# Optimization experiments

Measured on AMD Instinct MI355X. Metric: run time of the kernel, lower is better.

## Reference

```python
import jax, jax.numpy as jnp
import numpy as np

B, N, E = 8, 2048, 65536
NUM_RADIAL, H = 6, 128


def setup_inputs() -> dict:
    key = jax.random.key(0)
    ks = jax.random.split(key, 10)
    x = jax.random.normal(ks[0], (B, N, 1), dtype=jnp.float32)
    rbf = jax.random.normal(ks[1], (B, E, NUM_RADIAL), dtype=jnp.float32)
    i = jax.random.randint(ks[2], (E,), 0, N, dtype=jnp.int64)
    j = jax.random.randint(ks[3], (E,), 0, N, dtype=jnp.int64)
    # params (torch Linear convention: w [out, in], y = x @ w.T + b)
    emb_w = jax.random.uniform(ks[4], (H, 1), dtype=jnp.float32, minval=-np.sqrt(3), maxval=np.sqrt(3))
    emb_b = jax.random.normal(ks[5], (H,), dtype=jnp.float32) * 0.1
    rbf_w = jax.random.normal(ks[6], (H, NUM_RADIAL), dtype=jnp.float32) * (1.0 / np.sqrt(NUM_RADIAL))
    rbf_b = jax.random.normal(ks[7], (H,), dtype=jnp.float32) * 0.1
    lin_w = jax.random.normal(ks[8], (H, 3 * H), dtype=jnp.float32) * (1.0 / np.sqrt(3 * H))
    lin_b = jax.random.normal(ks[9], (H,), dtype=jnp.float32) * 0.1
    return {"x": x, "rbf": rbf, "i": i, "j": j,
            "emb_w": emb_w, "emb_b": emb_b,
            "rbf_w": rbf_w, "rbf_b": rbf_b,
            "lin_w": lin_w, "lin_b": lin_b}


def reference(x, rbf, i, j, emb_w, emb_b, rbf_w, rbf_b, lin_w, lin_b):
    act = jax.nn.silu
    # node embedding: [B, N, 1] -> [B, N, H]
    h = x @ emb_w.T + emb_b
    # rbf projection: [B, E, num_radial] -> [B, E, H]
    r = act(rbf @ rbf_w.T + rbf_b)
    # gather per-edge node features and concat: [B, E, 3H]
    cat = jnp.concatenate([h[:, i], h[:, j], r], axis=-1)
    # output: [B, E, H]
    return act(cat @ lin_w.T + lin_b)
```

## Files before the change

### kernel.cpp

```cpp
#include <hip/hip_runtime.h>

#define NB 8
#define NNODE 2048
#define NEDGE 65536
#define H 128
#define BM 64
#define RSTRIDE 132

typedef __attribute__((ext_vector_type(8))) short bf16x8;
typedef __attribute__((ext_vector_type(4))) float f32x4;

union U8 { uint4 u4; bf16x8 s8; };

__device__ __forceinline__ unsigned f32_bf16_rne(float f) {
    unsigned u = __float_as_uint(f);
    return (u + 0x7FFFu + ((u >> 16) & 1u)) >> 16;
}
__device__ __forceinline__ float bf16_f32(unsigned h) {
    return __uint_as_float(h << 16);
}
__device__ __forceinline__ float silu_f(float a) {
    return a / (1.0f + __expf(-a));
}

__global__ __launch_bounds__(64) void precomp_kernel(
    const float* __restrict__ emb_w, const float* __restrict__ emb_b,
    const float* __restrict__ lin_w, const float* __restrict__ lin_b,
    float* __restrict__ ws)
{
    const int bid = blockIdx.x;
    const int t = threadIdx.x;
    if (bid < 32) {
        const int ks = bid >> 3, nt = bid & 7;
        const int g = t >> 4, c = t & 15;
        const int col = nt * 16 + c;
        const float* src = lin_w + col * 384 + 256;
        uint4 w;
        {
            int k0 = ks * 32 + g * 8;
            w.x = f32_bf16_rne(src[k0 + 0]) | (f32_bf16_rne(src[k0 + 1]) << 16);
            w.y = f32_bf16_rne(src[k0 + 2]) | (f32_bf16_rne(src[k0 + 3]) << 16);
            w.z = f32_bf16_rne(src[k0 + 4]) | (f32_bf16_rne(src[k0 + 5]) << 16);
            w.w = f32_bf16_rne(src[k0 + 6]) | (f32_bf16_rne(src[k0 + 7]) << 16);
        }
        unsigned* w3f = (unsigned*)(ws + 384);
        *(uint4*)(w3f + bid * 256 + t * 4) = w;
    } else {
        const int o = (bid - 32) * 64 + t;
        const float* wrow = lin_w + o * 384;
        float u1 = 0.f, u2 = 0.f, v = lin_b[o];
        #pragma unroll 8
        for (int c = 0; c < 128; ++c) {
            float w1 = wrow[c], w2 = wrow[128 + c];
            u1 += emb_w[c] * w1;
            u2 += emb_w[c] * w2;
            v  += emb_b[c] * (w1 + w2);
        }
        ws[o] = u1; ws[128 + o] = u2; ws[256 + o] = v;
    }
}

__global__ __launch_bounds__(256, 4) void edge_kernel(
    const float* __restrict__ x,
    const float* __restrict__ rbf,
    const int*   __restrict__ gi,
    const int*   __restrict__ gj,
    const float* __restrict__ rbf_w,
    const float* __restrict__ rbf_b,
    const float* __restrict__ ws,
    float* __restrict__ out)
{
    __shared__ unsigned RHL[BM * RSTRIDE];
    __shared__ float rbf_s[BM * 6];

    const int tid  = threadIdx.x;
    const int wid  = tid >> 6;
    const int lane = tid & 63;
    const int g    = lane >> 4;
    const int c15  = lane & 15;
    const long m0  = (long)blockIdx.x * BM;

    if (tid < 96)
        ((float4*)rbf_s)[tid] = ((const float4*)(rbf + m0 * 6))[tid];

    float wa[8][6], wb[8];
    #pragma unroll
    for (int nt = 0; nt < 8; ++nt) {
        const int col = nt * 16 + c15;
        const float2* wp = (const float2*)(rbf_w + col * 6);
        float2 p0 = wp[0], p1 = wp[1], p2 = wp[2];
        wa[nt][0] = p0.x; wa[nt][1] = p0.y;
        wa[nt][2] = p1.x; wa[nt][3] = p1.y;
        wa[nt][4] = p2.x; wa[nt][5] = p2.y;
        wb[nt] = rbf_b[col];
    }
    __syncthreads();

    {
        float acc[8][4];
        #pragma unroll
        for (int nt = 0; nt < 8; ++nt)
            #pragma unroll
            for (int r = 0; r < 4; ++r) acc[nt][r] = wb[nt];

        #pragma unroll
        for (int r = 0; r < 4; ++r) {
            const int row = wid * 16 + g * 4 + r;
            const float* q = rbf_s + row * 6;
            const float q0 = q[0], q1 = q[1], q2 = q[2];
            const float q3 = q[3], q4 = q[4], q5 = q[5];
            #pragma unroll
            for (int nt = 0; nt < 8; ++nt) {
                float d = acc[nt][r];
                d += q0 * wa[nt][0]; d += q1 * wa[nt][1];
                d += q2 * wa[nt][2]; d += q3 * wa[nt][3];
                d += q4 * wa[nt][4]; d += q5 * wa[nt][5];
                acc[nt][r] = d;
            }
        }
        #pragma unroll
        for (int nt = 0; nt < 8; ++nt)
            #pragma unroll
            for (int r = 0; r < 4; ++r) {
                const int row = wid * 16 + g * 4 + r;
                float y = silu_f(acc[nt][r]);
                unsigned hi = f32_bf16_rne(y);
                unsigned lo = f32_bf16_rne(y - bf16_f32(hi));
                RHL[row * RSTRIDE + nt * 16 + c15] = hi | (lo << 16);
            }
    }
    __syncthreads();

    f32x4 acc4[8];
    #pragma unroll
    for (int nt = 0; nt < 8; ++nt) acc4[nt] = (f32x4){0.f, 0.f, 0.f, 0.f};

    const unsigned* w3f = (const unsigned*)(ws + 384);
    const int rrow = wid * 16 + c15;

    #pragma unroll
    for (int ks = 0; ks < 4; ++ks) {
        const unsigned* base = &RHL[rrow * RSTRIDE + ks * 32 + g * 8];
        uint4 wlo = *(const uint4*)base;
        uint4 whi = *(const uint4*)(base + 4);
        U8 Ah, Al;
        Ah.u4.x = (wlo.x & 0xFFFFu) | (wlo.y << 16);
        Ah.u4.y = (wlo.z & 0xFFFFu) | (wlo.w << 16);
        Ah.u4.z = (whi.x & 0xFFFFu) | (whi.y << 16);
        Ah.u4.w = (whi.z & 0xFFFFu) | (whi.w << 16);
        Al.u4.x = (wlo.x >> 16) | (wlo.y & 0xFFFF0000u);
        Al.u4.y = (wlo.z >> 16) | (wlo.w & 0xFFFF0000u);
        Al.u4.z = (whi.x >> 16) | (whi.y & 0xFFFF0000u);
        Al.u4.w = (whi.z >> 16) | (whi.w & 0xFFFF0000u);

        #pragma unroll
        for (int h = 0; h < 2; ++h) {
            U8 wf[4];
            #pragma unroll
            for (int q = 0; q < 4; ++q)
                wf[q].u4 = *(const uint4*)(w3f + ((ks * 8 + h * 4 + q) * 64 + lane) * 4);
            #pragma unroll
            for (int q = 0; q < 4; ++q) {
                const int nt = h * 4 + q;
                acc4[nt] = __builtin_amdgcn_mfma_f32_16x16x32_bf16(Ah.s8, wf[q].s8, acc4[nt], 0, 0, 0);
                acc4[nt] = __builtin_amdgcn_mfma_f32_16x16x32_bf16(Al.s8, wf[q].s8, acc4[nt], 0, 0, 0);
            }
        }
    }

    const int b = blockIdx.x >> 10;
    const float* xb = x + b * NNODE;
    const int ebase = ((blockIdx.x & 1023) << 6) + wid * 16 + g * 4;

    float sr[4], tr[4];
    #pragma unroll
    for (int r = 0; r < 4; ++r) {
        const int e = ebase + r;
        sr[r] = xb[gi[e]];
        tr[r] = xb[gj[e]];
    }

    #pragma unroll
    for (int nt = 0; nt < 8; ++nt) {
        const int col = nt * 16 + c15;
        const float u1c = ws[col], u2c = ws[128 + col], vc = ws[256 + col];
        const long mbase = m0 + wid * 16 + g * 4;
        #pragma unroll
        for (int r = 0; r < 4; ++r) {
            float o = acc4[nt][r] + sr[r] * u1c + tr[r] * u2c + vc;
            out[(mbase + r) * H + col] = silu_f(o);
        }
    }
}

extern "C" void kernel_launch(void* const* d_in, const int* in_sizes, int n_in,
                              void* d_out, int out_size, void* d_ws, size_t ws_size,
                              hipStream_t stream) {
    const float* x     = (const float*)d_in[0];
    const float* rbf   = (const float*)d_in[1];
    const int*   gi    = (const int*)  d_in[2];
    const int*   gj    = (const int*)  d_in[3];
    const float* emb_w = (const float*)d_in[4];
    const float* emb_b = (const float*)d_in[5];
    const float* rbf_w = (const float*)d_in[6];
    const float* rbf_b = (const float*)d_in[7];
    const float* lin_w = (const float*)d_in[8];
    const float* lin_b = (const float*)d_in[9];
    float* out = (float*)d_out;
    float* ws  = (float*)d_ws;

    precomp_kernel<<<34, 64, 0, stream>>>(emb_w, emb_b, lin_w, lin_b, ws);

    const int nblocks = (NB * NEDGE) / BM;
    edge_kernel<<<nblocks, 256, 0, stream>>>(x, rbf, gi, gj, rbf_w, rbf_b, ws, out);
}
```

Before: 361.5 us.

## Split hi/lo bf16 LDS planes, hoist gathers, and prefetch weight fragments

Each thread now computes 8 contiguous rbf-projection columns with vectorized weight loads. The hi and lo bf16 halves go into separate LDS arrays as packed uint4 stores, so the MFMA A operands are read directly without per-k-step repacking. The node-feature gathers (gi/gj index loads and x lookups) move to the start of the kernel, where their latency can overlap the rbf projection. B-operand weight fragments are double-buffered across k-steps. The intent is to hide global-load latency and cut ALU/LDS shuffle work, at the cost of more live registers, which may reduce occupancy.

```diff
diff --git a/kernel.cpp b/kernel.cpp
--- a/kernel.cpp
+++ b/kernel.cpp
@@ -5,7 +5,7 @@
 #define NEDGE 65536
 #define H 128
 #define BM 64
-#define RSTRIDE 132
+#define SH 68
 
 typedef __attribute__((ext_vector_type(8))) short bf16x8;
 typedef __attribute__((ext_vector_type(4))) float f32x4;
@@ -70,7 +70,8 @@
     const float* __restrict__ ws,
     float* __restrict__ out)
 {
-    __shared__ unsigned RHL[BM * RSTRIDE];
+    __shared__ unsigned RH[BM * SH];
+    __shared__ unsigned RL[BM * SH];
     __shared__ float rbf_s[BM * 6];
 
     const int tid  = threadIdx.x;
@@ -83,51 +84,59 @@
     if (tid < 96)
         ((float4*)rbf_s)[tid] = ((const float4*)(rbf + m0 * 6))[tid];
 
-    float wa[8][6], wb[8];
-    #pragma unroll
-    for (int nt = 0; nt < 8; ++nt) {
-        const int col = nt * 16 + c15;
-        const float2* wp = (const float2*)(rbf_w + col * 6);
-        float2 p0 = wp[0], p1 = wp[1], p2 = wp[2];
-        wa[nt][0] = p0.x; wa[nt][1] = p0.y;
-        wa[nt][2] = p1.x; wa[nt][3] = p1.y;
-        wa[nt][4] = p2.x; wa[nt][5] = p2.y;
-        wb[nt] = rbf_b[col];
+    const int ebase = ((int)(blockIdx.x & 1023) << 6) + wid * 16 + g * 4;
+    const int4 gi4 = *(const int4*)(gi + ebase);
+    const int4 gj4 = *(const int4*)(gj + ebase);
+    const float* xb = x + (blockIdx.x >> 10) * NNODE;
+    float sr[4], tr[4];
+    sr[0] = xb[gi4.x]; sr[1] = xb[gi4.y]; sr[2] = xb[gi4.z]; sr[3] = xb[gi4.w];
+    tr[0] = xb[gj4.x]; tr[1] = xb[gj4.y]; tr[2] = xb[gj4.z]; tr[3] = xb[gj4.w];
+
+    const unsigned* w3f = (const unsigned*)(ws + 384);
+    uint4 wf0[4], wf1[4];
+    #pragma unroll
+    for (int q = 0; q < 4; ++q)
+        wf0[q] = *(const uint4*)(w3f + ((0 * 8 + q) * 64 + lane) * 4);
+
+    float wa[48], wb[8];
+    {
+        const float4* wsrc = (const float4*)(rbf_w + c15 * 48);
+        #pragma unroll
+        for (int i = 0; i < 12; ++i)
+            *(float4*)&wa[i * 4] = wsrc[i];
+        *(float4*)&wb[0] = *(const float4*)(rbf_b + c15 * 8);
+        *(float4*)&wb[4] = *(const float4*)(rbf_b + c15 * 8 + 4);
     }
     __syncthreads();
 
-    {
-        float acc[8][4];
-        #pragma unroll
-        for (int nt = 0; nt < 8; ++nt)
+    #pragma unroll
+    for (int r = 0; r < 4; ++r) {
+        const int row = wid * 16 + g * 4 + r;
+        const float* qq = rbf_s + row * 6;
+        const float q0 = qq[0], q1 = qq[1], q2 = qq[2];
+        const float q3 = qq[3], q4 = qq[4], q5 = qq[5];
+        unsigned hp[4], lp[4];
+        #pragma unroll
+        for (int p = 0; p < 4; ++p) {
+            float y[2];
             #pragma unroll
-            for (int r = 0; r < 4; ++r) acc[nt][r] = wb[nt];
-
-        #pragma unroll
-        for (int r = 0; r < 4; ++r) {
-            const int row = wid * 16 + g * 4 + r;
-            const float* q = rbf_s + row * 6;
-            const float q0 = q[0], q1 = q[1], q2 = q[2];
-            const float q3 = q[3], q4 = q[4], q5 = q[5];
-            #pragma unroll
-            for (int nt = 0; nt < 8; ++nt) {
-                float d = acc[nt][r];
-                d += q0 * wa[nt][0]; d += q1 * wa[nt][1];
-                d += q2 * wa[nt][2]; d += q3 * wa[nt][3];
-                d += q4 * wa[nt][4]; d += q5 * wa[nt][5];
-                acc[nt][r] = d;
+            for (int s = 0; s < 2; ++s) {
+                const int nt = 2 * p + s;
+                float d = wb[nt];
+                d += q0 * wa[nt * 6 + 0]; d += q1 * wa[nt * 6 + 1];
+                d += q2 * wa[nt * 6 + 2]; d += q3 * wa[nt * 6 + 3];
+                d += q4 * wa[nt * 6 + 4]; d += q5 * wa[nt * 6 + 5];
+                y[s] = silu_f(d);
             }
-        }
-        #pragma unroll
-        for (int nt = 0; nt < 8; ++nt)
-            #pragma unroll
-            for (int r = 0; r < 4; ++r) {
-                const int row = wid * 16 + g * 4 + r;
-                float y = silu_f(acc[nt][r]);
-                unsigned hi = f32_bf16_rne(y);
-                unsigned lo = f32_bf16_rne(y - bf16_f32(hi));
-                RHL[row * RSTRIDE + nt * 16 + c15] = hi | (lo << 16);
-            }
+            const unsigned h0 = f32_bf16_rne(y[0]);
+            const unsigned l0 = f32_bf16_rne(y[0] - bf16_f32(h0));
+            const unsigned h1 = f32_bf16_rne(y[1]);
+            const unsigned l1 = f32_bf16_rne(y[1] - bf16_f32(h1));
+            hp[p] = h0 | (h1 << 16);
+            lp[p] = l0 | (l1 << 16);
+        }
+        *(uint4*)&RH[row * SH + c15 * 4] = make_uint4(hp[0], hp[1], hp[2], hp[3]);
+        *(uint4*)&RL[row * SH + c15 * 4] = make_uint4(lp[0], lp[1], lp[2], lp[3]);
     }
     __syncthreads();
 
@@ -135,49 +144,37 @@
     #pragma unroll
     for (int nt = 0; nt < 8; ++nt) acc4[nt] = (f32x4){0.f, 0.f, 0.f, 0.f};
 
-    const unsigned* w3f = (const unsigned*)(ws + 384);
-    const int rrow = wid * 16 + c15;
+    const int arow = wid * 16 + c15;
 
     #pragma unroll
     for (int ks = 0; ks < 4; ++ks) {
-        const unsigned* base = &RHL[rrow * RSTRIDE + ks * 32 + g * 8];
-        uint4 wlo = *(const uint4*)base;
-        uint4 whi = *(const uint4*)(base + 4);
         U8 Ah, Al;
-        Ah.u4.x = (wlo.x & 0xFFFFu) | (wlo.y << 16);
-        Ah.u4.y = (wlo.z & 0xFFFFu) | (wlo.w << 16);
-        Ah.u4.z = (whi.x & 0xFFFFu) | (whi.y << 16);
-        Ah.u4.w = (whi.z & 0xFFFFu) | (whi.w << 16);
-        Al.u4.x = (wlo.x >> 16) | (wlo.y & 0xFFFF0000u);
-        Al.u4.y = (wlo.z >> 16) | (wlo.w & 0xFFFF0000u);
-        Al.u4.z = (whi.x >> 16) | (whi.y & 0xFFFF0000u);
-        Al.u4.w = (whi.z >> 16) | (whi.w & 0xFFFF0000u);
-
-        #pragma unroll
-        for (int h = 0; h < 2; ++h) {
-            U8 wf[4];
+        Ah.u4 = *(const uint4*)&RH[arow * SH + ks * 16 + g * 4];
+        Al.u4 = *(const uint4*)&RL[arow * SH + ks * 16 + g * 4];
+
+        #pragma unroll
+        for (int q = 0; q < 4; ++q)
+            wf1[q] = *(const uint4*)(w3f + ((ks * 8 + 4 + q) * 64 + lane) * 4);
+
+        #pragma unroll
+        for (int q = 0; q < 4; ++q) {
+            U8 B; B.u4 = wf0[q];
+            acc4[q] = __builtin_amdgcn_mfma_f32_16x16x32_bf16(Ah.s8, B.s8, acc4[q], 0, 0, 0);
+            acc4[q] = __builtin_amdgcn_mfma_f32_16x16x32_bf16(Al.s8, B.s8, acc4[q], 0, 0, 0);
+        }
+
+        if (ks < 3) {
             #pragma unroll
             for (int q = 0; q < 4; ++q)
-                wf[q].u4 = *(const uint4*)(w3f + ((ks * 8 + h * 4 + q) * 64 + lane) * 4);
-            #pragma unroll
-            for (int q = 0; q < 4; ++q) {
-                const int nt = h * 4 + q;
-                acc4[nt] = __builtin_amdgcn_mfma_f32_16x16x32_bf16(Ah.s8, wf[q].s8, acc4[nt], 0, 0, 0);
-                acc4[nt] = __builtin_amdgcn_mfma_f32_16x16x32_bf16(Al.s8, wf[q].s8, acc4[nt], 0, 0, 0);
-            }
-        }
-    }
-
-    const int b = blockIdx.x >> 10;
-    const float* xb = x + b * NNODE;
-    const int ebase = ((blockIdx.x & 1023) << 6) + wid * 16 + g * 4;
-
-    float sr[4], tr[4];
-    #pragma unroll
-    for (int r = 0; r < 4; ++r) {
-        const int e = ebase + r;
-        sr[r] = xb[gi[e]];
-        tr[r] = xb[gj[e]];
+                wf0[q] = *(const uint4*)(w3f + (((ks + 1) * 8 + q) * 64 + lane) * 4);
+        }
+
+        #pragma unroll
+        for (int q = 0; q < 4; ++q) {
+            U8 B; B.u4 = wf1[q];
+            acc4[4 + q] = __builtin_amdgcn_mfma_f32_16x16x32_bf16(Ah.s8, B.s8, acc4[4 + q], 0, 0, 0);
+            acc4[4 + q] = __builtin_amdgcn_mfma_f32_16x16x32_bf16(Al.s8, B.s8, acc4[4 + q], 0, 0, 0);
+        }
     }
 
     #pragma unroll
```

Result: slower. 369.9 us (+2.3%).
